# Optimization experiments

Measured on AMD Instinct MI355X. Metric: run time of the kernel, lower is better.

The kernel has to match this reference:

```python
import jax, jax.numpy as jnp
import numpy as np

GAMMA = 0.25
GN_EPS = 1e-5


def setup_inputs() -> dict:
    key = jax.random.key(0)
    k1, k2, k3 = jax.random.split(key, 3)
    B, T, C = 16, 2048, 512
    G, V, Dv = 2, 320, 256
    x = jax.random.normal(k1, (B, T, C), dtype=jnp.float32)
    conv_w = jax.random.normal(k2, (G, C // G, C // G), dtype=jnp.float32) * 0.05
    gn_w = jnp.ones((C,), dtype=jnp.float32)
    gn_b = jnp.zeros((C,), dtype=jnp.float32)
    emb = 0.01 * jax.random.normal(k3, (V, G, Dv), dtype=jnp.float32)
    return {"x": x, "conv_w": conv_w, "gn_w": gn_w, "gn_b": gn_b, "emb": emb}


def _vq_forward(x, conv_w, gn_w, gn_b, emb):
    B, T, C = x.shape
    V, G, Dv = emb.shape
    sg = jax.lax.stop_gradient
    # time_first -> BxCxT
    xt = jnp.transpose(x, (0, 2, 1))  # [B,C,T]
    # grouped 1x1 conv (no bias)
    xg = xt.reshape(B, G, C // G, T)
    ze = jnp.einsum('goi,bgit->bgot', conv_w, xg)  # [B,G,C/G,T]
    # Fp32GroupNorm over (C/G, T) per group, biased variance
    zf = ze.astype(jnp.float32)
    mu = jnp.mean(zf, axis=(2, 3), keepdims=True)
    var = jnp.mean(jnp.square(zf - mu), axis=(2, 3), keepdims=True)
    zn = ((zf - mu) * jax.lax.rsqrt(var + GN_EPS)).reshape(B, C, T)
    ze = (zn * gn_w[None, :, None] + gn_b[None, :, None]).astype(ze.dtype)  # [B,C,T]
    # split into groups along feature dim: [B,T,G,Dv]
    ze_ = jnp.transpose(ze.reshape(B, G, Dv, T), (0, 3, 1, 2))
    # squared distances [V,B,T,G] (argmin of ||.||_2 == argmin of ||.||_2^2)
    d2 = (jnp.sum(jnp.square(ze_), axis=-1)[None]
          - 2.0 * jnp.einsum('btgd,vgd->vbtg', ze_, emb)
          + jnp.sum(jnp.square(emb), axis=-1)[:, None, None, :])
    idx = jnp.argmin(d2, axis=0)  # [B,T,G] int
    # gather nearest codewords per group
    zq = emb[idx, jnp.arange(G)[None, None, :]]  # [B,T,G,Dv]
    zq = jnp.transpose(zq.reshape(B, T, C), (0, 2, 1))  # [B,C,T]
    # straight-through
    out = sg(zq) + (ze - sg(ze))  # [B,C,T]
    # code perplexity (no grad)
    probs = jnp.mean(jax.nn.one_hot(sg(idx), V, dtype=jnp.float32), axis=(0, 1))  # [G,V]
    perplexity = jnp.sum(jnp.exp(-jnp.sum(probs * jnp.log(probs + 1e-7), axis=-1)))
    # losses
    zef, zqf = ze.astype(jnp.float32), zq.astype(jnp.float32)
    latent = jnp.mean(jnp.square(zqf - sg(zef)))
    commit = jnp.mean(jnp.square(zef - sg(zqf)))
    loss = latent + GAMMA * commit
    out = jnp.transpose(out, (0, 2, 1))  # back to BxTxC
    return out, loss, perplexity, idx


def reference(x, conv_w, gn_w, gn_b, emb):
    return _vq_forward(x, conv_w, gn_w, gn_b, emb)
```

## Files before the change

### kernel.cpp

```cpp
#include <hip/hip_runtime.h>

#define Bq 16
#define Tq 2048
#define Cq 512
#define Gq 2
#define CGq 256
#define Vq 320
#define Mq 32768
#define LOSS_OFF 16777216
#define PPL_OFF  16777217
#define IDX_OFF  16777218

#define MARGIN 1.75e-4f
#define LIST_CAP 16384
#define LIST2_CAP 1024

#define WS_PCONV 0
#define WS_PLOSS 16384
#define WS_MU    49152
#define WS_RS    49280
#define WS_E2    49408
#define WS_LOSSF 51968
#define WS_CNT   51976
#define WS_CNT2  51980
#define WS_HIST  51984
#define WS_PL2   54544
#define WS_LIST2 70928
#define WS_WSP   131072
#define WS_LISTQ 917504
#define WS_ESP   1048576

#define SL(X, r) ((X) * 16 + ((r) ^ ((X) & 7)))

typedef short s16x8 __attribute__((ext_vector_type(8)));
typedef float f32x4v __attribute__((ext_vector_type(4)));

__device__ __forceinline__ void bsplit(float x, unsigned &b1, unsigned &b2) {
    unsigned u = __float_as_uint(x);
    unsigned r1 = (u + 0x7fffu + ((u >> 16) & 1u)) & 0xffff0000u;
    b1 = r1 >> 16;
    float d = x - __uint_as_float(r1);
    unsigned u2 = __float_as_uint(d);
    b2 = (u2 + 0x7fffu + ((u2 >> 16) & 1u)) >> 16;
}

__device__ __forceinline__ void bsplit3(float x, unsigned &h, unsigned &m, unsigned &l) {
    unsigned u = __float_as_uint(x);
    unsigned r1 = (u + 0x7fffu + ((u >> 16) & 1u)) & 0xffff0000u;
    h = r1 >> 16;
    float d1 = x - __uint_as_float(r1);
    unsigned u2 = __float_as_uint(d1);
    unsigned r2 = (u2 + 0x7fffu + ((u2 >> 16) & 1u)) & 0xffff0000u;
    m = r2 >> 16;
    float d2 = d1 - __uint_as_float(r2);
    unsigned u3 = __float_as_uint(d2);
    l = (u3 + 0x7fffu + ((u3 >> 16) & 1u)) >> 16;
}

__global__ __launch_bounds__(256) void k_prep(const float* __restrict__ w,
                                              const float* __restrict__ emb,
                                              unsigned char* __restrict__ wsp,
                                              unsigned char* __restrict__ esp,
                                              float* __restrict__ e2w) {
    int bx = blockIdx.x, tid = threadIdx.x;
    if (bx < 64) {
        int t = bx * 256 + tid;
        int g = t >> 13, o = (t >> 5) & 255, ihi = t & 31;
        const float* src = w + ((size_t)(g * 256 + o)) * 256 + ihi * 8;
        float xv[8];
        *(float4*)(xv + 0) = *(const float4*)(src);
        *(float4*)(xv + 4) = *(const float4*)(src + 4);
        unsigned ph[4] = {0,0,0,0}, pm[4] = {0,0,0,0}, pl[4] = {0,0,0,0};
#pragma unroll
        for (int e = 0; e < 8; e++) {
            unsigned h, m, l;
            bsplit3(xv[e], h, m, l);
            ph[e >> 1] |= h << ((e & 1) * 16);
            pm[e >> 1] |= m << ((e & 1) * 16);
            pl[e >> 1] |= l << ((e & 1) * 16);
        }
        int kc = ihi >> 2, quad = ihi & 3, ct = o >> 4, lf = o & 15;
        size_t base = (size_t)(g * 3) * 131072 + (size_t)kc * 16384 + ct * 1024 + quad * 256 + lf * 16;
        *(uint4*)(wsp + base + 0 * 131072) = *(uint4*)ph;
        *(uint4*)(wsp + base + 1 * 131072) = *(uint4*)pm;
        *(uint4*)(wsp + base + 2 * 131072) = *(uint4*)pl;
    } else if (bx < 224) {
        int row  = (bx - 64) * 4 + (tid >> 6);
        int lane = tid & 63;
        float4 v = *(const float4*)(emb + (size_t)row * 256 + lane * 4);
        float s = v.x * v.x + v.y * v.y + v.z * v.z + v.w * v.w;
#pragma unroll
        for (int m = 1; m < 64; m <<= 1) s += __shfl_xor(s, m);
        if (lane == 0) e2w[(row & 1) * Vq + (row >> 1)] = s;
    } else {
        int t = (bx - 224) * 256 + tid;
        int g  = t / 10240;
        int r  = t - g * 10240;
        int kc = r / 1280;
        int r2 = r - kc * 1280;
        int ct = r2 >> 6;
        int r3 = r2 & 63;
        int kq = r3 >> 4, l15 = r3 & 15;
        int v  = ct * 16 + l15;
        int k0 = kc * 32 + kq * 8;
        const float* src = emb + ((size_t)v * 2 + g) * 256 + k0;
        float xv[8];
        *(float4*)(xv + 0) = *(const float4*)(src);
        *(float4*)(xv + 4) = *(const float4*)(src + 4);
        unsigned ph[4] = {0,0,0,0}, pl[4] = {0,0,0,0};
#pragma unroll
        for (int e = 0; e < 8; e++) {
            unsigned h, l;
            bsplit(xv[e], h, l);
            ph[e >> 1] |= h << ((e & 1) * 16);
            pl[e >> 1] |= l << ((e & 1) * 16);
        }
        size_t base = (size_t)g * 327680 + (size_t)kc * 20480
                    + (size_t)((ct * 4 + kq) * 16 + l15) * 16;
        *(uint4*)(esp + base) = *(uint4*)ph;
        *(uint4*)(esp + base + 163840) = *(uint4*)pl;
    }
}

__global__ __launch_bounds__(256, 2) void k_convM(const float* __restrict__ x,
    const unsigned char* __restrict__ wsp, float* __restrict__ ze,
    double* __restrict__ pconv)
{
    __shared__ unsigned char lds[73728];
    __shared__ double reds[4], redq[4];
    uint4* Bs = (uint4*)lds;
    uint4* As = (uint4*)(lds + 49152);

    int tid = threadIdx.x, bx = blockIdx.x;
    int mt = bx >> 1, g = bx & 1;
    int m0 = mt * 128;
    int w = tid >> 6, lane = tid & 63;
    int quad = lane >> 4, l15 = lane & 15;
    int arow = tid >> 1, ah = tid & 1;
    int aw = arow >> 5, art = (arow >> 4) & 1, ar = arow & 15;
    const float* xrow = x + (size_t)(m0 + arow) * Cq + g * CGq + ah * 16;
    const unsigned char* wslab = wsp + (size_t)(g * 3) * 131072;

    f32x4v zero4 = {0.f, 0.f, 0.f, 0.f};
    f32x4v acc[2][16];
#pragma unroll
    for (int i = 0; i < 2; i++)
#pragma unroll
        for (int j = 0; j < 16; j++) acc[i][j] = zero4;

    for (int kc = 0; kc < 8; kc++) {
        if (kc) __syncthreads();
#pragma unroll
        for (int j = 0; j < 12; j++) {
            int L = (w * 12 + j) * 1024 + lane * 16;
            int p = L >> 14, r = L & 16383;
            __builtin_amdgcn_global_load_lds(
                (const __attribute__((address_space(1))) void*)(wslab + (size_t)p * 131072 + (size_t)kc * 16384 + r),
                (__attribute__((address_space(3))) void*)(lds + L), 16, 0, 0);
        }
        float xv[16];
        *(float4*)(xv + 0)  = *(const float4*)(xrow + kc * 32 + 0);
        *(float4*)(xv + 4)  = *(const float4*)(xrow + kc * 32 + 4);
        *(float4*)(xv + 8)  = *(const float4*)(xrow + kc * 32 + 8);
        *(float4*)(xv + 12) = *(const float4*)(xrow + kc * 32 + 12);
#pragma unroll
        for (int ii = 0; ii < 2; ii++) {
            unsigned ph[4] = {0,0,0,0}, pm[4] = {0,0,0,0}, pl[4] = {0,0,0,0};
#pragma unroll
            for (int e = 0; e < 8; e++) {
                unsigned h, m, l;
                bsplit3(xv[ii * 8 + e], h, m, l);
                ph[e >> 1] |= h << ((e & 1) * 16);
                pm[e >> 1] |= m << ((e & 1) * 16);
                pl[e >> 1] |= l << ((e & 1) * 16);
            }
            int aq = ah * 2 + ii;
            As[SL(((0 * 4 + aw) * 2 + art) * 4 + aq, ar)] = *(uint4*)ph;
            As[SL(((1 * 4 + aw) * 2 + art) * 4 + aq, ar)] = *(uint4*)pm;
            As[SL(((2 * 4 + aw) * 2 + art) * 4 + aq, ar)] = *(uint4*)pl;
        }
        __syncthreads();
        s16x8 afr[3][2];
#pragma unroll
        for (int p = 0; p < 3; p++)
#pragma unroll
            for (int rt = 0; rt < 2; rt++)
                afr[p][rt] = __builtin_bit_cast(s16x8,
                    As[SL(((p * 4 + w) * 2 + rt) * 4 + quad, l15)]);
#pragma unroll
        for (int ct = 0; ct < 16; ct++) {
            s16x8 b0 = __builtin_bit_cast(s16x8, Bs[0 * 1024 + ct * 64 + quad * 16 + l15]);
            s16x8 b1 = __builtin_bit_cast(s16x8, Bs[1 * 1024 + ct * 64 + quad * 16 + l15]);
            s16x8 b2 = __builtin_bit_cast(s16x8, Bs[2 * 1024 + ct * 64 + quad * 16 + l15]);
#pragma unroll
            for (int rt = 0; rt < 2; rt++) {
                acc[rt][ct] = __builtin_amdgcn_mfma_f32_16x16x32_bf16(afr[0][rt], b0, acc[rt][ct], 0, 0, 0);
                acc[rt][ct] = __builtin_amdgcn_mfma_f32_16x16x32_bf16(afr[1][rt], b0, acc[rt][ct], 0, 0, 0);
                acc[rt][ct] = __builtin_amdgcn_mfma_f32_16x16x32_bf16(afr[2][rt], b0, acc[rt][ct], 0, 0, 0);
                acc[rt][ct] = __builtin_amdgcn_mfma_f32_16x16x32_bf16(afr[0][rt], b1, acc[rt][ct], 0, 0, 0);
                acc[rt][ct] = __builtin_amdgcn_mfma_f32_16x16x32_bf16(afr[1][rt], b1, acc[rt][ct], 0, 0, 0);
                acc[rt][ct] = __builtin_amdgcn_mfma_f32_16x16x32_bf16(afr[0][rt], b2, acc[rt][ct], 0, 0, 0);
            }
        }
    }

    float s = 0.f, q = 0.f;
    float* zb = ze + (size_t)m0 * Cq + g * CGq;
#pragma unroll
    for (int rt = 0; rt < 2; rt++)
#pragma unroll
    for (int ct = 0; ct < 16; ct++)
#pragma unroll
    for (int j = 0; j < 4; j++) {
        float v = acc[rt][ct][j];
        zb[(size_t)(w * 32 + rt * 16 + quad * 4 + j) * Cq + ct * 16 + l15] = v;
        s += v;
        q = __builtin_fmaf(v, v, q);
    }
    double ds = (double)s, dq = (double)q;
#pragma unroll
    for (int m = 1; m < 64; m <<= 1) { ds += __shfl_xor(ds, m); dq += __shfl_xor(dq, m); }
    if (lane == 0) { reds[w] = ds; redq[w] = dq; }
    __syncthreads();
    if (tid == 0) {
        pconv[bx * 2 + 0] = reds[0] + reds[1] + reds[2] + reds[3];
        pconv[bx * 2 + 1] = redq[0] + redq[1] + redq[2] + redq[3];
    }
}

__global__ __launch_bounds__(256) void k_stats(const double* __restrict__ pconv,
                                               float* __restrict__ muw,
                                               float* __restrict__ rsw) {
    int tid = threadIdx.x;
    int bg = tid >> 3, r = tid & 7;
    int b = bg >> 1, g = bg & 1;
    double s = 0.0, q = 0.0;
    for (int j = r; j < 16; j += 8) {
        int pi = (b * 16 + j) * 2 + g;
        s += pconv[pi * 2 + 0];
        q += pconv[pi * 2 + 1];
    }
#pragma unroll
    for (int m = 1; m < 8; m <<= 1) { s += __shfl_xor(s, m); q += __shfl_xor(q, m); }
    if (r == 0) {
        double mu = s / 524288.0;
        double var = q / 524288.0 - mu * mu;
        double rs = 1.0 / sqrt(var + 1e-5);
        muw[bg] = (float)mu;
        rsw[bg] = (float)rs;
    }
}

__global__ __launch_bounds__(256, 2) void k_distA(const unsigned char* __restrict__ esp,
    const float* __restrict__ gw, const float* __restrict__ gb,
    const float* __restrict__ muw, const float* __restrict__ rsw,
    const float* __restrict__ e2w, float* dout,
    unsigned* __restrict__ cntw, unsigned* __restrict__ cnt2w,
    unsigned long long* __restrict__ listq, unsigned* __restrict__ list2,
    unsigned* __restrict__ hist, double* __restrict__ ploss)
{
    __shared__ uint4 Asl[1024];
    __shared__ unsigned char ldsB[40960];
    __shared__ float e2s[Vq];
    __shared__ float z2l[128];
    __shared__ double redp[4];
    uint4* Bsl = (uint4*)ldsB;

    int tid = threadIdx.x, bx = blockIdx.x;
    int mt = bx >> 1, g = bx & 1;
    int m0 = mt * 128;
    int bg = (m0 >> 11) * 2 + g;
    float muf = muw[bg], rsf = rsw[bg];
    int w = tid >> 6, lane = tid & 63;
    int quad = lane >> 4, l15 = lane & 15;

    for (int i = tid; i < Vq; i += 256) e2s[i] = e2w[g * Vq + i];

    int arow = tid >> 1, ah = tid & 1;
    int aw = arow >> 5, art = (arow >> 4) & 1, ar = arow & 15;
    const float* zrow = dout + (size_t)m0 * Cq + g * CGq + (size_t)arow * Cq;
    const unsigned char* eslab = esp + (size_t)g * 327680;

    f32x4v zero4 = {0.f, 0.f, 0.f, 0.f};
    f32x4v acc[2][20];
#pragma unroll
    for (int i = 0; i < 2; i++)
#pragma unroll
        for (int j = 0; j < 20; j++) acc[i][j] = zero4;
    float z2acc = 0.f;

    for (int kc8 = 0; kc8 < 8; kc8++) {
        if (kc8) __syncthreads();
        int k0 = kc8 * 32;
#pragma unroll
        for (int j = 0; j < 10; j++) {
            int L = j * 4096 + tid * 16;
            int s = (j >= 5) ? 1 : 0;
            __builtin_amdgcn_global_load_lds(
                (const __attribute__((address_space(1))) void*)(eslab + (size_t)s * 143360 + (size_t)kc8 * 20480 + L),
                (__attribute__((address_space(3))) void*)(ldsB + L), 16, 0, 0);
        }
#pragma unroll
        for (int i2 = 0; i2 < 2; i2++) {
            uint4 o1, o2;
            unsigned hw[4], lw[4];
#pragma unroll
            for (int ii = 0; ii < 2; ii++) {
                int koff = k0 + ah * 16 + i2 * 8 + ii * 4;
                float4 z  = *(const float4*)(zrow + koff);
                float4 gv = *(const float4*)(gw + g * CGq + koff);
                float4 bvv= *(const float4*)(gb + g * CGq + koff);
                float zn0 = (z.x - muf) * rsf * gv.x + bvv.x;
                float zn1 = (z.y - muf) * rsf * gv.y + bvv.y;
                float zn2 = (z.z - muf) * rsf * gv.z + bvv.z;
                float zn3 = (z.w - muf) * rsf * gv.w + bvv.w;
                z2acc = __builtin_fmaf(zn0, zn0, z2acc);
                z2acc = __builtin_fmaf(zn1, zn1, z2acc);
                z2acc = __builtin_fmaf(zn2, zn2, z2acc);
                z2acc = __builtin_fmaf(zn3, zn3, z2acc);
                unsigned h0,l0,h1,l1,h2,l2,h3,l3;
                bsplit(zn0, h0, l0); bsplit(zn1, h1, l1);
                bsplit(zn2, h2, l2); bsplit(zn3, h3, l3);
                hw[ii*2+0] = h0 | (h1 << 16); hw[ii*2+1] = h2 | (h3 << 16);
                lw[ii*2+0] = l0 | (l1 << 16); lw[ii*2+1] = l2 | (l3 << 16);
            }
            o1.x = hw[0]; o1.y = hw[1]; o1.z = hw[2]; o1.w = hw[3];
            o2.x = lw[0]; o2.y = lw[1]; o2.z = lw[2]; o2.w = lw[3];
            int kq = ah * 2 + i2;
            Asl[SL(((0*4 + aw)*2 + art)*4 + kq, ar)] = o1;
            Asl[SL(((1*4 + aw)*2 + art)*4 + kq, ar)] = o2;
        }
        __syncthreads();
        s16x8 afr[2][2];
#pragma unroll
        for (int s = 0; s < 2; s++)
#pragma unroll
            for (int rt = 0; rt < 2; rt++)
                afr[s][rt] = __builtin_bit_cast(s16x8,
                    Asl[SL(((s*4 + w)*2 + rt)*4 + quad, l15)]);
#pragma unroll
        for (int ct = 0; ct < 20; ct++) {
            s16x8 b0 = __builtin_bit_cast(s16x8, Bsl[((0*20 + ct)*4 + quad)*16 + l15]);
            s16x8 b1 = __builtin_bit_cast(s16x8, Bsl[((1*20 + ct)*4 + quad)*16 + l15]);
#pragma unroll
            for (int rt = 0; rt < 2; rt++) {
                acc[rt][ct] = __builtin_amdgcn_mfma_f32_16x16x32_bf16(afr[0][rt], b0, acc[rt][ct], 0, 0, 0);
                acc[rt][ct] = __builtin_amdgcn_mfma_f32_16x16x32_bf16(afr[0][rt], b1, acc[rt][ct], 0, 0, 0);
                acc[rt][ct] = __builtin_amdgcn_mfma_f32_16x16x32_bf16(afr[1][rt], b0, acc[rt][ct], 0, 0, 0);
            }
        }
    }

    {
        float z2pair = z2acc + __shfl_xor(z2acc, 1);
        if (ah == 0) z2l[arow] = z2pair;
    }
    __syncthreads();

    double lacc = 0.0;
#pragma unroll
    for (int rt = 0; rt < 2; rt++)
#pragma unroll
    for (int j = 0; j < 4; j++) {
        float m1 = 3.402823466e+38f; int i1 = 0;
#pragma unroll
        for (int ct = 0; ct < 20; ct++) {
            float d2a = e2s[ct * 16 + l15] - 2.0f * acc[rt][ct][j];
            if (d2a < m1) { m1 = d2a; i1 = ct * 16 + l15; }
        }
#pragma unroll
        for (int mm = 1; mm < 16; mm <<= 1) {
            float ov = __shfl_xor(m1, mm);
            int   oi = __shfl_xor(i1, mm);
            if (ov < m1 || (ov == m1 && oi < i1)) { m1 = ov; i1 = oi; }
        }
        float thr = m1 + MARGIN;
        unsigned mask = 0;
#pragma unroll
        for (int ct = 0; ct < 20; ct++) {
            float d2a = e2s[ct * 16 + l15] - 2.0f * acc[rt][ct][j];
            if (d2a <= thr) mask |= (1u << ct);
        }
        int cnt = __popc(mask);
#pragma unroll
        for (int mm = 1; mm < 16; mm <<= 1) cnt += __shfl_xor(cnt, mm);
        int mrow = m0 + w * 32 + rt * 16 + quad * 4 + j;
        unsigned q = (unsigned)mrow * 2u + (unsigned)g;
        unsigned flag = 0;
        if (cnt > 1) {
            if ((i1 & 15) == l15) mask &= ~(1u << (i1 >> 4));
            int cl2 = __popc(mask);
            int inc = cl2;
#pragma unroll
            for (int off = 1; off < 16; off <<= 1) {
                int t = __shfl_up(inc, off, 16);
                if (l15 >= off) inc += t;
            }
            int pre = inc - cl2;
            if (cnt <= 5) {
                int pos_ = 0;
                if (l15 == 0) pos_ = (int)atomicAdd(cntw, 1u);
                pos_ = __shfl(pos_, 0, 16);
                if ((unsigned)pos_ < LIST_CAP) {
                    flag = 512u;
                    unsigned long long contrib = 0ull;
                    unsigned mm2 = mask; int k = pre;
                    while (mm2) {
                        int ct2 = __ffs(mm2) - 1; mm2 &= mm2 - 1;
                        contrib |= ((unsigned long long)(unsigned)(ct2 * 16 + l15)) << (20 + 9 * k);
                        k++;
                    }
#pragma unroll
                    for (int mm = 1; mm < 16; mm <<= 1)
                        contrib |= __shfl_xor(contrib, mm);
                    if (l15 == 0)
                        listq[pos_] = (unsigned long long)q
                                    | ((unsigned long long)(unsigned)cnt << 17) | contrib;
                }
            } else {
                if (l15 == 0) {
                    unsigned p2 = atomicAdd(cnt2w, 1u);
                    if (p2 < LIST2_CAP) { list2[p2] = q; flag = 512u; }
                }
            }
        }
        if (l15 == 0) {
            if (flag) {
                dout[IDX_OFF + q] = __uint_as_float((unsigned)i1 | flag);
            } else {
                dout[IDX_OFF + q] = (float)i1;
                atomicAdd(&hist[g * Vq + i1], 1u);
                lacc += (double)z2l[mrow - m0] + (double)m1;
            }
        }
    }
#pragma unroll
    for (int mm = 1; mm < 64; mm <<= 1) lacc += __shfl_xor(lacc, mm);
    if (lane == 0) redp[w] = lacc;
    __syncthreads();
    if (tid == 0) ploss[bx] = redp[0] + redp[1] + redp[2] + redp[3];
}

__global__ __launch_bounds__(256) void k_exF(const float* __restrict__ emb,
    const float* __restrict__ gw, const float* __restrict__ gb,
    const float* __restrict__ muw, const float* __restrict__ rsw,
    const float* __restrict__ e2w, float* dout,
    unsigned* __restrict__ hist, double* __restrict__ ploss2,
    const unsigned long long* __restrict__ listq, const unsigned* __restrict__ cntw,
    double* __restrict__ lossf,
    const unsigned* __restrict__ cnt2w, const unsigned* __restrict__ list2)
{
    int tid = threadIdx.x, lane = tid & 63;
    int gwid = blockIdx.x * 4 + (tid >> 6);
    int cslot = lane >> 2, j = lane & 3;
    unsigned nn = *cntw; if (nn > LIST_CAP) nn = LIST_CAP;
    int n = (int)nn;
    double lacc = 0.0;
    for (int it = gwid; it < n; it += 2048) {
        unsigned long long e = listq[it];
        unsigned q = (unsigned)(e & 0x1FFFFull);
        int cnt = (int)((e >> 17) & 7u);
        int m = (int)(q >> 1), g = (int)(q & 1u);
        int bg = (m >> 11) * 2 + g;
        float muf = muw[bg], rsf = rsw[bg];
        int v = (int)(__float_as_uint(dout[IDX_OFF + q]) & 511u);
        if (cslot >= 1 && cslot < cnt)
            v = (int)((e >> (20 + 9 * (cslot - 1))) & 511ull);
        const float* zb  = dout + (size_t)m * Cq + g * CGq;
        const float* gwb = gw + g * CGq;
        const float* gbb = gb + g * CGq;
        const float* eb  = emb + ((size_t)v * Gq + g) * CGq;
        float z2p = 0.f, dp = 0.f;
        for (int kc = 0; kc < 16; kc++) {
            int k0 = kc * 16 + j * 4;
            float4 z  = *(const float4*)(zb + k0);
            float4 gv = *(const float4*)(gwb + k0);
            float4 bv = *(const float4*)(gbb + k0);
            float4 e4 = *(const float4*)(eb + k0);
            float zn0 = __fadd_rn(__fmul_rn(__fmul_rn(__fsub_rn(z.x, muf), rsf), gv.x), bv.x);
            float zn1 = __fadd_rn(__fmul_rn(__fmul_rn(__fsub_rn(z.y, muf), rsf), gv.y), bv.y);
            float zn2 = __fadd_rn(__fmul_rn(__fmul_rn(__fsub_rn(z.z, muf), rsf), gv.z), bv.z);
            float zn3 = __fadd_rn(__fmul_rn(__fmul_rn(__fsub_rn(z.w, muf), rsf), gv.w), bv.w);
            z2p = __builtin_fmaf(zn0, zn0, z2p);
            z2p = __builtin_fmaf(zn1, zn1, z2p);
            z2p = __builtin_fmaf(zn2, zn2, z2p);
            z2p = __builtin_fmaf(zn3, zn3, z2p);
            dp = __builtin_fmaf(zn0, e4.x, dp);
            dp = __builtin_fmaf(zn1, e4.y, dp);
            dp = __builtin_fmaf(zn2, e4.z, dp);
            dp = __builtin_fmaf(zn3, e4.w, dp);
        }
        z2p += __shfl_xor(z2p, 1); z2p += __shfl_xor(z2p, 2);
        dp  += __shfl_xor(dp, 1);  dp  += __shfl_xor(dp, 2);
        float d2 = __fadd_rn(__fsub_rn(z2p, 2.0f * dp), e2w[g * Vq + v]);
#pragma unroll
        for (int mm = 4; mm < 64; mm <<= 1) {
            float od = __shfl_xor(d2, mm);
            int   ov = __shfl_xor(v, mm);
            if (od < d2 || (od == d2 && ov < v)) { d2 = od; v = ov; }
        }
        if (lane == 0) {
            dout[IDX_OFF + q] = (float)v;
            atomicAdd(&hist[g * Vq + v], 1u);
            lacc += (double)d2;
        }
    }
    if (lane == 0) ploss2[gwid] = lacc;

    unsigned nn2 = *cnt2w; if (nn2 > LIST2_CAP) nn2 = LIST2_CAP;
    int n2 = (int)nn2;
    for (int it = gwid; it < n2; it += 2048) {
        int q = (int)list2[it];
        int m = q >> 1, g = q & 1;
        int bg = (m >> 11) * 2 + g;
        float muf = muw[bg], rsf = rsw[bg];
        const float* zb = dout + (size_t)m * Cq + g * CGq;
        int k0 = lane * 4;
        float4 z  = *(const float4*)(zb + k0);
        float4 gv = *(const float4*)(gw + g * CGq + k0);
        float4 bv = *(const float4*)(gb + g * CGq + k0);
        float zn0 = __fadd_rn(__fmul_rn(__fmul_rn(__fsub_rn(z.x, muf), rsf), gv.x), bv.x);
        float zn1 = __fadd_rn(__fmul_rn(__fmul_rn(__fsub_rn(z.y, muf), rsf), gv.y), bv.y);
        float zn2 = __fadd_rn(__fmul_rn(__fmul_rn(__fsub_rn(z.z, muf), rsf), gv.z), bv.z);
        float zn3 = __fadd_rn(__fmul_rn(__fmul_rn(__fsub_rn(z.w, muf), rsf), gv.w), bv.w);
        float s = 0.f;
        for (int kc = 0; kc < 16; kc++) {
            int src = (lane & 3) + kc * 4;
            float a0 = __shfl(zn0, src), a1 = __shfl(zn1, src);
            float a2 = __shfl(zn2, src), a3 = __shfl(zn3, src);
            s = __builtin_fmaf(a0, a0, s);
            s = __builtin_fmaf(a1, a1, s);
            s = __builtin_fmaf(a2, a2, s);
            s = __builtin_fmaf(a3, a3, s);
        }
        s += __shfl_xor(s, 1); s += __shfl_xor(s, 2);
        float z2 = s;
        float m1 = 3.402823466e+38f; int i1 = 0;
        for (int v = 0; v < Vq; v += 2) {
            const float* e0 = emb + ((size_t)v * Gq + g) * CGq + k0;
            float4 ea = *(const float4*)e0;
            float4 eb4 = *(const float4*)(e0 + Gq * CGq);
            float da = zn0 * ea.x;  da = __builtin_fmaf(zn1, ea.y, da);
            da = __builtin_fmaf(zn2, ea.z, da); da = __builtin_fmaf(zn3, ea.w, da);
            float db = zn0 * eb4.x; db = __builtin_fmaf(zn1, eb4.y, db);
            db = __builtin_fmaf(zn2, eb4.z, db); db = __builtin_fmaf(zn3, eb4.w, db);
#pragma unroll
            for (int mm = 1; mm < 64; mm <<= 1) { da += __shfl_xor(da, mm); db += __shfl_xor(db, mm); }
            float d2a = __fadd_rn(__fsub_rn(z2, 2.0f * da), e2w[g * Vq + v]);
            float d2b = __fadd_rn(__fsub_rn(z2, 2.0f * db), e2w[g * Vq + v + 1]);
            if (d2a < m1) { m1 = d2a; i1 = v; }
            if (d2b < m1) { m1 = d2b; i1 = v + 1; }
        }
        if (lane == 0) {
            dout[IDX_OFF + q] = (float)i1;
            atomicAdd(&hist[g * Vq + i1], 1u);
            atomicAdd(lossf, (double)m1);
        }
    }
}

__global__ __launch_bounds__(256) void k_out(const float* __restrict__ emb, float* dout) {
    size_t u = (size_t)blockIdx.x * 256 + threadIdx.x;
    size_t pos = u * 4;
    int m = (int)(pos >> 9);
    int c = (int)(pos & 511);
    int g = c >> 8, d = c & 255;
    int v = (int)dout[IDX_OFF + (size_t)m * Gq + g];
    float4 o = *(const float4*)(emb + ((size_t)(v * 2 + g)) * 256 + d);
    *(float4*)(dout + pos) = o;
}

__global__ __launch_bounds__(256) void k_final(const double* __restrict__ ploss,
                                               const double* __restrict__ ploss2,
                                               const double* __restrict__ lossf,
                                               const unsigned* __restrict__ hist,
                                               float* dout) {
    __shared__ double redl[4], red0[4], red1[4];
    int tid = threadIdx.x;
    double s = 0.0;
    for (int i = tid; i < 512; i += 256) s += ploss[i];
    for (int i = tid; i < 2048; i += 256) s += ploss2[i];
#pragma unroll
    for (int m = 1; m < 64; m <<= 1) s += __shfl_xor(s, m);
    double e0 = 0.0, e1 = 0.0;
    for (int pid = tid; pid < 640; pid += 256) {
        double p = (double)hist[pid] * (1.0 / 32768.0);
        double t = p * log(p + 1e-7);
        if (pid < 320) e0 += t; else e1 += t;
    }
#pragma unroll
    for (int m = 1; m < 64; m <<= 1) { e0 += __shfl_xor(e0, m); e1 += __shfl_xor(e1, m); }
    int lane = tid & 63, wv_ = tid >> 6;
    if (lane == 0) { redl[wv_] = s; red0[wv_] = e0; red1[wv_] = e1; }
    __syncthreads();
    if (tid == 0) {
        double S  = redl[0] + redl[1] + redl[2] + redl[3] + *lossf;
        double E0 = red0[0] + red0[1] + red0[2] + red0[3];
        double E1 = red1[0] + red1[1] + red1[2] + red1[3];
        dout[LOSS_OFF] = (float)(1.25 * S / 16777216.0);
        dout[PPL_OFF]  = (float)(exp(-E0) + exp(-E1));
    }
}

extern "C" void kernel_launch(void* const* d_in, const int* in_sizes, int n_in,
                              void* d_out, int out_size, void* d_ws, size_t ws_size,
                              hipStream_t stream) {
    const float* x   = (const float*)d_in[0];
    const float* w   = (const float*)d_in[1];
    const float* gw  = (const float*)d_in[2];
    const float* gb  = (const float*)d_in[3];
    const float* emb = (const float*)d_in[4];
    float* dout = (float*)d_out;
    char* ws = (char*)d_ws;
    double* pconv   = (double*)(ws + WS_PCONV);
    double* ploss   = (double*)(ws + WS_PLOSS);
    float* muw      = (float*)(ws + WS_MU);
    float* rsw      = (float*)(ws + WS_RS);
    float* e2w      = (float*)(ws + WS_E2);
    double* lossf   = (double*)(ws + WS_LOSSF);
    unsigned* cntw  = (unsigned*)(ws + WS_CNT);
    unsigned* cnt2w = (unsigned*)(ws + WS_CNT2);
    unsigned* hist  = (unsigned*)(ws + WS_HIST);
    double* ploss2  = (double*)(ws + WS_PL2);
    unsigned* list2 = (unsigned*)(ws + WS_LIST2);
    unsigned char* wsp = (unsigned char*)(ws + WS_WSP);
    unsigned long long* listq = (unsigned long long*)(ws + WS_LISTQ);
    unsigned char* esp = (unsigned char*)(ws + WS_ESP);

    hipMemsetAsync(ws + WS_LOSSF, 0, 2576, stream);
    k_prep<<<304, 256, 0, stream>>>(w, emb, wsp, esp, e2w);
    k_convM<<<512, 256, 0, stream>>>(x, wsp, dout, pconv);
    k_stats<<<1, 256, 0, stream>>>(pconv, muw, rsw);
    k_distA<<<512, 256, 0, stream>>>(esp, gw, gb, muw, rsw, e2w, dout,
                                     cntw, cnt2w, listq, list2, hist, ploss);
    k_exF<<<512, 256, 0, stream>>>(emb, gw, gb, muw, rsw, e2w, dout, hist, ploss2,
                                   listq, cntw, lossf, cnt2w, list2);
    k_out<<<16384, 256, 0, stream>>>(emb, dout);
    k_final<<<1, 256, 0, stream>>>(ploss, ploss2, lossf, hist, dout);
}
```

Baseline: 160.7 us.

## Fuse codeword gather into distance kernels and halve distA row tile

Removes the separate k_out gather kernel. Each row's nearest codeword is now written straight into the output by k_distA for resolved rows, and by k_exF for rows that needed exact refinement. k_distA also moves from 128-row to 64-row tiles with twice the blocks and a launch bound raised to 3, aiming for more occupancy and less accumulator register pressure. The trade-off is that the embedding B slab is loaded into LDS twice as often per row, and the loop keeps a leftover redundant z load.

```diff
diff --git a/kernel.cpp b/kernel.cpp
--- a/kernel.cpp
+++ b/kernel.cpp
@@ -251,24 +251,25 @@
     }
 }
 
-__global__ __launch_bounds__(256, 2) void k_distA(const unsigned char* __restrict__ esp,
+__global__ __launch_bounds__(256, 3) void k_distA(const unsigned char* __restrict__ esp,
     const float* __restrict__ gw, const float* __restrict__ gb,
     const float* __restrict__ muw, const float* __restrict__ rsw,
-    const float* __restrict__ e2w, float* dout,
+    const float* __restrict__ e2w, const float* __restrict__ emb, float* dout,
     unsigned* __restrict__ cntw, unsigned* __restrict__ cnt2w,
     unsigned long long* __restrict__ listq, unsigned* __restrict__ list2,
     unsigned* __restrict__ hist, double* __restrict__ ploss)
 {
-    __shared__ uint4 Asl[1024];
+    __shared__ uint4 Asl[512];
     __shared__ unsigned char ldsB[40960];
     __shared__ float e2s[Vq];
-    __shared__ float z2l[128];
+    __shared__ float z2l[64];
+    __shared__ unsigned idxl[64];
     __shared__ double redp[4];
     uint4* Bsl = (uint4*)ldsB;
 
     int tid = threadIdx.x, bx = blockIdx.x;
     int mt = bx >> 1, g = bx & 1;
-    int m0 = mt * 128;
+    int m0 = mt * 64;
     int bg = (m0 >> 11) * 2 + g;
     float muf = muw[bg], rsf = rsw[bg];
     int w = tid >> 6, lane = tid & 63;
@@ -276,17 +277,15 @@
 
     for (int i = tid; i < Vq; i += 256) e2s[i] = e2w[g * Vq + i];
 
-    int arow = tid >> 1, ah = tid & 1;
-    int aw = arow >> 5, art = (arow >> 4) & 1, ar = arow & 15;
-    const float* zrow = dout + (size_t)m0 * Cq + g * CGq + (size_t)arow * Cq;
+    int arow = tid >> 2, akq = tid & 3;
+    int awt = arow >> 4, ar = arow & 15;
+    const float* zrow = dout + (size_t)(m0 + arow) * Cq + g * CGq + akq * 8;
     const unsigned char* eslab = esp + (size_t)g * 327680;
 
     f32x4v zero4 = {0.f, 0.f, 0.f, 0.f};
-    f32x4v acc[2][20];
-#pragma unroll
-    for (int i = 0; i < 2; i++)
-#pragma unroll
-        for (int j = 0; j < 20; j++) acc[i][j] = zero4;
+    f32x4v acc[20];
+#pragma unroll
+    for (int j = 0; j < 20; j++) acc[j] = zero4;
     float z2acc = 0.f;
 
     for (int kc8 = 0; kc8 < 8; kc8++) {
@@ -300,20 +299,20 @@
                 (const __attribute__((address_space(1))) void*)(eslab + (size_t)s * 143360 + (size_t)kc8 * 20480 + L),
                 (__attribute__((address_space(3))) void*)(ldsB + L), 16, 0, 0);
         }
-#pragma unroll
-        for (int i2 = 0; i2 < 2; i2++) {
-            uint4 o1, o2;
+        {
             unsigned hw[4], lw[4];
 #pragma unroll
             for (int ii = 0; ii < 2; ii++) {
-                int koff = k0 + ah * 16 + i2 * 8 + ii * 4;
-                float4 z  = *(const float4*)(zrow + koff);
+                int koff = k0 + akq * 8 + ii * 4;
+                float4 z  = *(const float4*)(zrow + kc8 * 0 + koff - akq * 8 + akq * 8);
+                (void)z;
+                float4 zz = *(const float4*)(dout + (size_t)(m0 + arow) * Cq + g * CGq + koff);
                 float4 gv = *(const float4*)(gw + g * CGq + koff);
                 float4 bvv= *(const float4*)(gb + g * CGq + koff);
-                float zn0 = (z.x - muf) * rsf * gv.x + bvv.x;
-                float zn1 = (z.y - muf) * rsf * gv.y + bvv.y;
-                float zn2 = (z.z - muf) * rsf * gv.z + bvv.z;
-                float zn3 = (z.w - muf) * rsf * gv.w + bvv.w;
+                float zn0 = (zz.x - muf) * rsf * gv.x + bvv.x;
+                float zn1 = (zz.y - muf) * rsf * gv.y + bvv.y;
+                float zn2 = (zz.z - muf) * rsf * gv.z + bvv.z;
+                float zn3 = (zz.w - muf) * rsf * gv.w + bvv.w;
                 z2acc = __builtin_fmaf(zn0, zn0, z2acc);
                 z2acc = __builtin_fmaf(zn1, zn1, z2acc);
                 z2acc = __builtin_fmaf(zn2, zn2, z2acc);
@@ -324,48 +323,39 @@
                 hw[ii*2+0] = h0 | (h1 << 16); hw[ii*2+1] = h2 | (h3 << 16);
                 lw[ii*2+0] = l0 | (l1 << 16); lw[ii*2+1] = l2 | (l3 << 16);
             }
+            uint4 o1, o2;
             o1.x = hw[0]; o1.y = hw[1]; o1.z = hw[2]; o1.w = hw[3];
             o2.x = lw[0]; o2.y = lw[1]; o2.z = lw[2]; o2.w = lw[3];
-            int kq = ah * 2 + i2;
-            Asl[SL(((0*4 + aw)*2 + art)*4 + kq, ar)] = o1;
-            Asl[SL(((1*4 + aw)*2 + art)*4 + kq, ar)] = o2;
+            Asl[SL((0 * 4 + awt) * 4 + akq, ar)] = o1;
+            Asl[SL((1 * 4 + awt) * 4 + akq, ar)] = o2;
         }
         __syncthreads();
-        s16x8 afr[2][2];
-#pragma unroll
-        for (int s = 0; s < 2; s++)
-#pragma unroll
-            for (int rt = 0; rt < 2; rt++)
-                afr[s][rt] = __builtin_bit_cast(s16x8,
-                    Asl[SL(((s*4 + w)*2 + rt)*4 + quad, l15)]);
+        s16x8 ah_ = __builtin_bit_cast(s16x8, Asl[SL((0 * 4 + w) * 4 + quad, l15)]);
+        s16x8 al_ = __builtin_bit_cast(s16x8, Asl[SL((1 * 4 + w) * 4 + quad, l15)]);
 #pragma unroll
         for (int ct = 0; ct < 20; ct++) {
-            s16x8 b0 = __builtin_bit_cast(s16x8, Bsl[((0*20 + ct)*4 + quad)*16 + l15]);
-            s16x8 b1 = __builtin_bit_cast(s16x8, Bsl[((1*20 + ct)*4 + quad)*16 + l15]);
-#pragma unroll
-            for (int rt = 0; rt < 2; rt++) {
-                acc[rt][ct] = __builtin_amdgcn_mfma_f32_16x16x32_bf16(afr[0][rt], b0, acc[rt][ct], 0, 0, 0);
-                acc[rt][ct] = __builtin_amdgcn_mfma_f32_16x16x32_bf16(afr[0][rt], b1, acc[rt][ct], 0, 0, 0);
-                acc[rt][ct] = __builtin_amdgcn_mfma_f32_16x16x32_bf16(afr[1][rt], b0, acc[rt][ct], 0, 0, 0);
-            }
+            s16x8 b0 = __builtin_bit_cast(s16x8, Bsl[(ct * 4 + quad) * 16 + l15]);
+            s16x8 b1 = __builtin_bit_cast(s16x8, Bsl[1280 + (ct * 4 + quad) * 16 + l15]);
+            acc[ct] = __builtin_amdgcn_mfma_f32_16x16x32_bf16(ah_, b0, acc[ct], 0, 0, 0);
+            acc[ct] = __builtin_amdgcn_mfma_f32_16x16x32_bf16(ah_, b1, acc[ct], 0, 0, 0);
+            acc[ct] = __builtin_amdgcn_mfma_f32_16x16x32_bf16(al_, b0, acc[ct], 0, 0, 0);
         }
     }
 
     {
-        float z2pair = z2acc + __shfl_xor(z2acc, 1);
-        if (ah == 0) z2l[arow] = z2pair;
+        float z2p = z2acc + __shfl_xor(z2acc, 1);
+        z2p += __shfl_xor(z2p, 2);
+        if (akq == 0) z2l[arow] = z2p;
     }
     __syncthreads();
 
     double lacc = 0.0;
-#pragma unroll
-    for (int rt = 0; rt < 2; rt++)
 #pragma unroll
     for (int j = 0; j < 4; j++) {
         float m1 = 3.402823466e+38f; int i1 = 0;
 #pragma unroll
         for (int ct = 0; ct < 20; ct++) {
-            float d2a = e2s[ct * 16 + l15] - 2.0f * acc[rt][ct][j];
+            float d2a = e2s[ct * 16 + l15] - 2.0f * acc[ct][j];
             if (d2a < m1) { m1 = d2a; i1 = ct * 16 + l15; }
         }
 #pragma unroll
@@ -378,13 +368,13 @@
         unsigned mask = 0;
 #pragma unroll
         for (int ct = 0; ct < 20; ct++) {
-            float d2a = e2s[ct * 16 + l15] - 2.0f * acc[rt][ct][j];
+            float d2a = e2s[ct * 16 + l15] - 2.0f * acc[ct][j];
             if (d2a <= thr) mask |= (1u << ct);
         }
         int cnt = __popc(mask);
 #pragma unroll
         for (int mm = 1; mm < 16; mm <<= 1) cnt += __shfl_xor(cnt, mm);
-        int mrow = m0 + w * 32 + rt * 16 + quad * 4 + j;
+        int mrow = m0 + w * 16 + quad * 4 + j;
         unsigned q = (unsigned)mrow * 2u + (unsigned)g;
         unsigned flag = 0;
         if (cnt > 1) {
@@ -425,8 +415,10 @@
             }
         }
         if (l15 == 0) {
+            unsigned packed = (unsigned)i1 | flag;
+            idxl[mrow - m0] = packed;
             if (flag) {
-                dout[IDX_OFF + q] = __uint_as_float((unsigned)i1 | flag);
+                dout[IDX_OFF + q] = __uint_as_float(packed);
             } else {
                 dout[IDX_OFF + q] = (float)i1;
                 atomicAdd(&hist[g * Vq + i1], 1u);
@@ -439,6 +431,18 @@
     if (lane == 0) redp[w] = lacc;
     __syncthreads();
     if (tid == 0) ploss[bx] = redp[0] + redp[1] + redp[2] + redp[3];
+
+#pragma unroll
+    for (int it = 0; it < 16; it++) {
+        int pos = it * 1024 + tid * 4;
+        int row = pos >> 8, d = pos & 255;
+        unsigned packed = idxl[row];
+        if (!(packed & 512u)) {
+            int v = (int)(packed & 511u);
+            float4 o = *(const float4*)(emb + ((size_t)(v * 2 + g)) * 256 + d);
+            *(float4*)(dout + (size_t)(m0 + row) * Cq + g * CGq + d) = o;
+        }
+    }
 }
 
 __global__ __launch_bounds__(256) void k_exF(const float* __restrict__ emb,
@@ -504,6 +508,10 @@
             atomicAdd(&hist[g * Vq + v], 1u);
             lacc += (double)d2;
         }
+        {
+            float4 o = *(const float4*)(emb + ((size_t)(v * 2 + g)) * 256 + lane * 4);
+            *(float4*)(dout + (size_t)m * Cq + g * CGq + lane * 4) = o;
+        }
     }
     if (lane == 0) ploss2[gwid] = lacc;
 
@@ -556,18 +564,11 @@
             atomicAdd(&hist[g * Vq + i1], 1u);
             atomicAdd(lossf, (double)m1);
         }
-    }
-}
-
-__global__ __launch_bounds__(256) void k_out(const float* __restrict__ emb, float* dout) {
-    size_t u = (size_t)blockIdx.x * 256 + threadIdx.x;
-    size_t pos = u * 4;
-    int m = (int)(pos >> 9);
-    int c = (int)(pos & 511);
-    int g = c >> 8, d = c & 255;
-    int v = (int)dout[IDX_OFF + (size_t)m * Gq + g];
-    float4 o = *(const float4*)(emb + ((size_t)(v * 2 + g)) * 256 + d);
-    *(float4*)(dout + pos) = o;
+        {
+            float4 o = *(const float4*)(emb + ((size_t)(i1 * 2 + g)) * 256 + lane * 4);
+            *(float4*)(dout + (size_t)m * Cq + g * CGq + lane * 4) = o;
+        }
+    }
 }
 
 __global__ __launch_bounds__(256) void k_final(const double* __restrict__ ploss,
@@ -578,7 +579,7 @@
     __shared__ double redl[4], red0[4], red1[4];
     int tid = threadIdx.x;
     double s = 0.0;
-    for (int i = tid; i < 512; i += 256) s += ploss[i];
+    for (int i = tid; i < 1024; i += 256) s += ploss[i];
     for (int i = tid; i < 2048; i += 256) s += ploss2[i];
 #pragma unroll
     for (int m = 1; m < 64; m <<= 1) s += __shfl_xor(s, m);
@@ -631,10 +632,9 @@
     k_prep<<<304, 256, 0, stream>>>(w, emb, wsp, esp, e2w);
     k_convM<<<512, 256, 0, stream>>>(x, wsp, dout, pconv);
     k_stats<<<1, 256, 0, stream>>>(pconv, muw, rsw);
-    k_distA<<<512, 256, 0, stream>>>(esp, gw, gb, muw, rsw, e2w, dout,
-                                     cntw, cnt2w, listq, list2, hist, ploss);
+    k_distA<<<1024, 256, 0, stream>>>(esp, gw, gb, muw, rsw, e2w, emb, dout,
+                                      cntw, cnt2w, listq, list2, hist, ploss);
     k_exF<<<512, 256, 0, stream>>>(emb, gw, gb, muw, rsw, e2w, dout, hist, ploss2,
                                    listq, cntw, lossf, cnt2w, list2);
-    k_out<<<16384, 256, 0, stream>>>(emb, dout);
     k_final<<<1, 256, 0, stream>>>(ploss, ploss2, lossf, hist, dout);
 }
```

Measured after the change: 165.1 us. 2.8% more time.

## Fuse codeword gather output into distance and exact-refine kernels, drop k_out

Applied to the files above, without the earlier changes.

Removes the separate k_out pass that re-read the stored indices and gathered codewords into the output. k_distA now keeps per-row packed indices in LDS and, after its reductions, writes the gathered codewords for rows it resolved. k_exF writes them for the rows it refines. The goal is to save a kernel launch and the extra index reads, and to overlap the large output store with distance work. In exchange, k_distA needs more LDS and stores, and correctness relies on flagged rows keeping their z values until k_exF reads them.

```diff
diff --git a/kernel.cpp b/kernel.cpp
--- a/kernel.cpp
+++ b/kernel.cpp
@@ -254,7 +254,7 @@
 __global__ __launch_bounds__(256, 2) void k_distA(const unsigned char* __restrict__ esp,
     const float* __restrict__ gw, const float* __restrict__ gb,
     const float* __restrict__ muw, const float* __restrict__ rsw,
-    const float* __restrict__ e2w, float* dout,
+    const float* __restrict__ e2w, const float* __restrict__ emb, float* dout,
     unsigned* __restrict__ cntw, unsigned* __restrict__ cnt2w,
     unsigned long long* __restrict__ listq, unsigned* __restrict__ list2,
     unsigned* __restrict__ hist, double* __restrict__ ploss)
@@ -263,6 +263,7 @@
     __shared__ unsigned char ldsB[40960];
     __shared__ float e2s[Vq];
     __shared__ float z2l[128];
+    __shared__ unsigned idxl[128];
     __shared__ double redp[4];
     uint4* Bsl = (uint4*)ldsB;
 
@@ -425,8 +426,10 @@
             }
         }
         if (l15 == 0) {
+            unsigned packed = (unsigned)i1 | flag;
+            idxl[mrow - m0] = packed;
             if (flag) {
-                dout[IDX_OFF + q] = __uint_as_float((unsigned)i1 | flag);
+                dout[IDX_OFF + q] = __uint_as_float(packed);
             } else {
                 dout[IDX_OFF + q] = (float)i1;
                 atomicAdd(&hist[g * Vq + i1], 1u);
@@ -439,6 +442,18 @@
     if (lane == 0) redp[w] = lacc;
     __syncthreads();
     if (tid == 0) ploss[bx] = redp[0] + redp[1] + redp[2] + redp[3];
+
+#pragma unroll
+    for (int it = 0; it < 32; it++) {
+        int pos = it * 1024 + tid * 4;
+        int row = pos >> 8, d = pos & 255;
+        unsigned packed = idxl[row];
+        if (!(packed & 512u)) {
+            int v = (int)(packed & 511u);
+            float4 o = *(const float4*)(emb + ((size_t)(v * 2 + g)) * 256 + d);
+            *(float4*)(dout + (size_t)(m0 + row) * Cq + g * CGq + d) = o;
+        }
+    }
 }
 
 __global__ __launch_bounds__(256) void k_exF(const float* __restrict__ emb,
@@ -504,6 +519,10 @@
             atomicAdd(&hist[g * Vq + v], 1u);
             lacc += (double)d2;
         }
+        {
+            float4 o = *(const float4*)(emb + ((size_t)(v * 2 + g)) * 256 + lane * 4);
+            *(float4*)(dout + (size_t)m * Cq + g * CGq + lane * 4) = o;
+        }
     }
     if (lane == 0) ploss2[gwid] = lacc;
 
@@ -556,18 +575,11 @@
             atomicAdd(&hist[g * Vq + i1], 1u);
             atomicAdd(lossf, (double)m1);
         }
-    }
-}
-
-__global__ __launch_bounds__(256) void k_out(const float* __restrict__ emb, float* dout) {
-    size_t u = (size_t)blockIdx.x * 256 + threadIdx.x;
-    size_t pos = u * 4;
-    int m = (int)(pos >> 9);
-    int c = (int)(pos & 511);
-    int g = c >> 8, d = c & 255;
-    int v = (int)dout[IDX_OFF + (size_t)m * Gq + g];
-    float4 o = *(const float4*)(emb + ((size_t)(v * 2 + g)) * 256 + d);
-    *(float4*)(dout + pos) = o;
+        {
+            float4 o = *(const float4*)(emb + ((size_t)(i1 * 2 + g)) * 256 + lane * 4);
+            *(float4*)(dout + (size_t)m * Cq + g * CGq + lane * 4) = o;
+        }
+    }
 }
 
 __global__ __launch_bounds__(256) void k_final(const double* __restrict__ ploss,
@@ -631,10 +643,9 @@
     k_prep<<<304, 256, 0, stream>>>(w, emb, wsp, esp, e2w);
     k_convM<<<512, 256, 0, stream>>>(x, wsp, dout, pconv);
     k_stats<<<1, 256, 0, stream>>>(pconv, muw, rsw);
-    k_distA<<<512, 256, 0, stream>>>(esp, gw, gb, muw, rsw, e2w, dout,
+    k_distA<<<512, 256, 0, stream>>>(esp, gw, gb, muw, rsw, e2w, emb, dout,
                                      cntw, cnt2w, listq, list2, hist, ploss);
     k_exF<<<512, 256, 0, stream>>>(emb, gw, gb, muw, rsw, e2w, dout, hist, ploss2,
                                    listq, cntw, lossf, cnt2w, list2);
-    k_out<<<16384, 256, 0, stream>>>(emb, dout);
     k_final<<<1, 256, 0, stream>>>(ploss, ploss2, lossf, hist, dout);
 }
```

Measured after the change: 156.4 us. 2.7% less time.
